# Performance work log

Measured on AMD Instinct MI355X. Metric: run time of the kernel, lower is better.

The kernel has to match this reference:

```python
import jax, jax.numpy as jnp
from jax import lax
import numpy as np

N, C, H, W = 8, 32, 64, 64
KS, NB = 7, 6            # kernel_size, num_bases
TB = (KS // 2) * NB      # total_bases = 18
BC = TB * NB             # bc_dim = 108
INTER = max(64, BC // 2) # 64
OUT = 64
PAD = KS // 2
EPS = 1e-5


def conv3x3(x, w, b):
    # x: (N,Cin,H,W), w: (Cout,Cin,3,3)
    y = lax.conv_general_dilated(x, w, (1, 1), [(1, 1), (1, 1)],
                                 dimension_numbers=('NCHW', 'OIHW', 'NCHW'))
    return y + b[None, :, None, None]


def batchnorm(x, g, b):
    # training-mode BN: batch stats over (N,H,W)
    mu = jnp.mean(x, axis=(0, 2, 3), keepdims=True)
    var = jnp.var(x, axis=(0, 2, 3), keepdims=True)
    return (x - mu) * lax.rsqrt(var + EPS) * g[None, :, None, None] + b[None, :, None, None]


def setup_inputs() -> dict:
    key = jax.random.key(0)
    ks = jax.random.split(key, 12)
    s = 0.05
    # random bases as in get_random_bases: (TB, KS*KS), zero-mean-ish rows
    f = jax.random.normal(ks[0], (TB, KS * KS), dtype=jnp.float32)
    bases = f - jnp.mean(f, axis=1, keepdims=True) / jnp.std(f, axis=1, keepdims=True)
    return {
        'x': jax.random.normal(ks[1], (N, C, H, W), dtype=jnp.float32),
        'conv1_w': jax.random.normal(ks[2], (INTER, C, 3, 3), dtype=jnp.float32) * s,
        'conv1_b': jax.random.normal(ks[3], (INTER,), dtype=jnp.float32) * s,
        'bn1_g': jnp.ones((INTER,), jnp.float32),
        'bn1_b': jnp.zeros((INTER,), jnp.float32),
        'conv2_w': jax.random.normal(ks[4], (BC, INTER, 3, 3), dtype=jnp.float32) * s,
        'conv2_b': jax.random.normal(ks[5], (BC,), dtype=jnp.float32) * s,
        'bn2_g': jnp.ones((BC,), jnp.float32),
        'bn2_b': jnp.zeros((BC,), jnp.float32),
        'bases': bases,
        'out_w': jax.random.normal(ks[6], (OUT, C * NB), dtype=jnp.float32) * s,
        'out_b': jax.random.normal(ks[7], (OUT,), dtype=jnp.float32) * s,
    }


def reference(x, conv1_w, conv1_b, bn1_g, bn1_b, conv2_w, conv2_b,
              bn2_g, bn2_b, bases, out_w, out_b):
    # bases_net: conv3x3 -> BN -> tanh -> conv3x3 -> BN -> tanh
    h = jnp.tanh(batchnorm(conv3x3(x, conv1_w, conv1_b), bn1_g, bn1_b))
    coef = jnp.tanh(batchnorm(conv3x3(h, conv2_w, conv2_b), bn2_g, bn2_b))
    # (N, BC, H, W) -> (N, NB, TB, H, W) -> (N, H, W, NB, TB)
    coef = coef.reshape(N, NB, TB, H, W).transpose(0, 3, 4, 1, 2)
    # atoms: (coef[...,None] * bases).sum(-2).transpose(-1,-2) => (N,H,W,KS^2,NB)
    atoms = jnp.einsum('nhwmt,tk->nhwkm', coef, bases)
    # unfold: channel-major (C, ks, ks) flattened, matching F.unfold
    patches = lax.conv_general_dilated_patches(
        x, (KS, KS), (1, 1), [(PAD, PAD), (PAD, PAD)],
        dimension_numbers=('NCHW', 'OIHW', 'NCHW'))  # (N, C*KS*KS, H, W)
    patches = patches.reshape(N, C, KS * KS, H, W)
    # per-pixel contraction over ks^2: (N,H,W,C,NB)
    bases_out = jnp.einsum('nckhw,nhwkm->nhwcm', patches, atoms)
    bases_out = bases_out.reshape(N, H, W, C * NB)
    out = jnp.einsum('nhwd,od->nohw', bases_out, out_w) + out_b[None, :, None, None]
    return out
```

## Files before the change

### kernel.cpp

```cpp
#include <hip/hip_runtime.h>
#include <hip/hip_bf16.h>

#define N_ 8
#define C_ 32
#define H_ 64
#define W_ 64
#define HW_ (H_*W_)
#define NHW_ (N_*HW_)
#define INTER_ 64
#define BC_ 108
#define KS_ 7
#define K2_ (KS_*KS_)
#define NB_ 6
#define TB_ 18
#define OUT_ 64
#define DDIM_ (C_*NB_)
#define P2CH_ 288

typedef __attribute__((ext_vector_type(8))) short short8;
typedef __attribute__((ext_vector_type(4))) float f32x4;
typedef __attribute__((ext_vector_type(2))) float f32x2;

__device__ __forceinline__ unsigned short f2bf(float f) {
    union { float f; unsigned u; } v; v.f = f;
    unsigned r = v.u + 0x7fffu + ((v.u >> 16) & 1u);
    return (unsigned short)(r >> 16);
}
__device__ __forceinline__ float bf2f(unsigned short h) {
    return __uint_as_float((unsigned int)h << 16);
}

__device__ __forceinline__ short8 frag4(const unsigned int* p) {
    union { unsigned int u[4]; short8 s; } v;
    v.u[0] = p[0]; v.u[1] = p[1]; v.u[2] = p[2]; v.u[3] = p[3];
    return v.s;
}

template<int TP0, int NTP>
__device__ __forceinline__ void pconv_pass(const float (*sx)[44],
                                           const float* __restrict__ bases,
                                           unsigned int* __restrict__ P2,
                                           int n, int c, int r0, int rb, int lane) {
    f32x2 av[NTP][4];
    #pragma unroll
    for (int tp = 0; tp < NTP; tp++)
        #pragma unroll
        for (int rr = 0; rr < 4; rr++) av[tp][rr] = (f32x2){0.f, 0.f};

    #pragma unroll 1
    for (int kx = 0; kx < 7; kx++) {
        float rw[12];
        const float* sp = &sx[lane + kx][rb];
        #pragma unroll
        for (int qq = 0; qq < 3; qq++) {
            float4 r4 = *(const float4*)(sp + qq * 4);
            rw[qq * 4 + 0] = r4.x; rw[qq * 4 + 1] = r4.y;
            rw[qq * 4 + 2] = r4.z; rw[qq * 4 + 3] = r4.w;
        }
        #pragma unroll
        for (int tp = 0; tp < NTP; tp++) {
            #pragma unroll
            for (int ky = 0; ky < 7; ky++) {
                f32x2 w2;
                w2.x = bases[(2 * (TP0 + tp)) * K2_ + ky * 7 + kx];
                w2.y = bases[(2 * (TP0 + tp) + 1) * K2_ + ky * 7 + kx];
                #pragma unroll
                for (int rr = 0; rr < 4; rr++) {
                    float xv = rw[rr + ky];
                    f32x2 xv2 = (f32x2){xv, xv};
                    av[tp][rr] += xv2 * w2;
                }
            }
        }
    }

    #pragma unroll
    for (int tp = 0; tp < NTP; tp++)
        #pragma unroll
        for (int rr = 0; rr < 4; rr++) {
            int gr = r0 + rb + rr;
            unsigned int pk = (unsigned int)f2bf(av[tp][rr].x) |
                              ((unsigned int)f2bf(av[tp][rr].y) << 16);
            P2[(((size_t)n * P2CH_ + (TP0 + tp) * 32 + c) << 12) + (gr << 6) + lane] = pk;
        }
}

__global__ __launch_bounds__(256) void k_prep(const float* __restrict__ w1,
                                              const float* __restrict__ w2,
                                              const float* __restrict__ ow,
                                              unsigned short* __restrict__ wb1,
                                              unsigned short* __restrict__ wb2,
                                              unsigned short* __restrict__ wbp,
                                              float* __restrict__ pz) {
    int bid = blockIdx.x, t = threadIdx.x;
    if (bid < 72) {
        int i = bid * 256 + t;
        int ci = i & 31, co = (i >> 5) & 63, s = i >> 11;
        wb1[i] = f2bf(w1[((co << 5) + ci) * 9 + s]);
    } else if (bid < 360) {
        int i = (bid - 72) * 256 + t;
        int ci = i & 63, co = (i >> 6) & 127, s = i >> 13;
        unsigned short v = 0;
        if (co < BC_) v = f2bf(w2[((co << 6) + ci) * 9 + s]);
        wb2[i] = v;
    } else if (bid < 408) {
        int i = (bid - 360) * 256 + t;
        if (i < OUT_ * DDIM_) {
            float v = ow[i];
            unsigned short hi = f2bf(v);
            wbp[i] = hi;
            wbp[OUT_ * DDIM_ + i] = f2bf(v - bf2f(hi));
        }
    } else {
        for (int i = t; i < (INTER_ + BC_) * 8 * 2; i += 256) pz[i] = 0.f;
    }
}

__global__ __launch_bounds__(256) void k_front(const float* __restrict__ x,
                                               const float* __restrict__ bases,
                                               const unsigned short* __restrict__ wb1,
                                               const float* __restrict__ b1,
                                               unsigned int* __restrict__ P2,
                                               float* __restrict__ y1,
                                               float2* __restrict__ part1) {
    __shared__ __align__(16) char smem[16896];
    int bid = blockIdx.x, t = threadIdx.x;

    if (bid < 1024) {
        float (*sx)[44] = (float(*)[44])smem;
        int rq = bid & 3;
        int c  = (bid >> 2) & 31;
        int n  = bid >> 7;
        int lane = t & 63, wv = t >> 6;
        int r0 = rq << 4;

        const float* xc = x + (((size_t)n * C_ + c) << 12);
        #pragma unroll
        for (int j = 0; j < 6; j++) {
            int p = wv + 4 * j;
            if (p < 22) {
                int grow = r0 - 3 + p;
                bool rowok = (grow >= 0 && grow < H_);
                int wx = lane - 3;
                float v = 0.f;
                if (rowok && wx >= 0) v = xc[(grow << 6) + wx];
                sx[lane][p] = v;
                if (lane < 6) {
                    int wx2 = 61 + lane;
                    float v2 = 0.f;
                    if (rowok && wx2 < W_) v2 = xc[(grow << 6) + wx2];
                    sx[64 + lane][p] = v2;
                }
            }
        }
        __syncthreads();

        int rb = wv * 4;
        pconv_pass<0, 5>(sx, bases, P2, n, c, r0, rb, lane);
        pconv_pass<5, 4>(sx, bases, P2, n, c, r0, rb, lane);
    } else {
        unsigned short* sx1 = (unsigned short*)smem;
        float* sbp = (float*)(sx1 + 198 * 40);

        int cid = bid - 1024;
        int n = cid >> 7;
        int rem = cid & 127;
        int co0 = (rem & 1) << 5;
        int h0 = rem >> 1;
        int lane = t & 63, wv = t >> 6;
        int q = lane >> 4, n15 = lane & 15;

        for (int e = t; e < 1536; e += 256) {
            int c = e & 31, rc4 = e >> 5;
            int r = rc4 >> 4, cq = rc4 & 15;
            int hh = h0 - 1 + r;
            bool rok = (hh >= 0 && hh < H_);
            float4 v = {0.f, 0.f, 0.f, 0.f};
            if (rok) v = *(const float4*)(x + (((size_t)n * C_ + c) << 12) + (hh << 6) + cq * 4);
            unsigned short* d = sx1 + (r * 66 + 1 + cq * 4) * 40 + c;
            d[0]   = f2bf(v.x);
            d[40]  = f2bf(v.y);
            d[80]  = f2bf(v.z);
            d[120] = f2bf(v.w);
        }
        if (t < 96) {
            int c = t & 31, r = t >> 5;
            sx1[(r * 66 + 0) * 40 + c] = 0;
            sx1[(r * 66 + 65) * 40 + c] = 0;
        }
        __syncthreads();

        f32x4 acc[2];
        acc[0] = (f32x4){0.f, 0.f, 0.f, 0.f};
        acc[1] = (f32x4){0.f, 0.f, 0.f, 0.f};
        #pragma unroll
        for (int s = 0; s < 9; s++) {
            int dy = s / 3, dx = s % 3;
            short8 bfr = *(const short8*)(sx1 + (dy * 66 + wv * 16 + n15 + dx) * 40 + q * 8);
            #pragma unroll
            for (int mt = 0; mt < 2; mt++) {
                short8 afr = *(const short8*)(wb1 + s * 2048 + (co0 + mt * 16 + n15) * 32 + q * 8);
                acc[mt] = __builtin_amdgcn_mfma_f32_16x16x32_bf16(afr, bfr, acc[mt], 0, 0, 0);
            }
        }

        int wcol = wv * 16 + n15;
        float sa[2][4], sa2[2][4];
        #pragma unroll
        for (int mt = 0; mt < 2; mt++)
            #pragma unroll
            for (int reg = 0; reg < 4; reg++) {
                int co = co0 + mt * 16 + q * 4 + reg;
                float v = acc[mt][reg] + b1[co];
                y1[(((size_t)n * INTER_ + co) << 12) + (h0 << 6) + wcol] = v;
                sa[mt][reg] = v; sa2[mt][reg] = v * v;
            }
        #pragma unroll
        for (int mt = 0; mt < 2; mt++)
            #pragma unroll
            for (int reg = 0; reg < 4; reg++) {
                float s = sa[mt][reg], s2 = sa2[mt][reg];
                #pragma unroll
                for (int off = 1; off < 16; off <<= 1) {
                    s += __shfl_xor(s, off);
                    s2 += __shfl_xor(s2, off);
                }
                if (n15 == 0) {
                    int cl = mt * 16 + q * 4 + reg;
                    sbp[wv * 64 + cl * 2] = s;
                    sbp[wv * 64 + cl * 2 + 1] = s2;
                }
            }
        __syncthreads();
        if (t < 32) {
            float s = 0.f, s2 = 0.f;
            #pragma unroll
            for (int w = 0; w < 4; w++) { s += sbp[w * 64 + t * 2]; s2 += sbp[w * 64 + t * 2 + 1]; }
            atomicAdd(&part1[((co0 + t) << 3) + n].x, s);
            atomicAdd(&part1[((co0 + t) << 3) + n].y, s2);
        }
    }
}

template<int CIN, int COG, int ROWS, int WPAD, int NCOQ>
__global__ __launch_bounds__(256) void k_conv3(const unsigned short* __restrict__ xb,
                                               const unsigned short* __restrict__ wb,
                                               const float* __restrict__ bias,
                                               float* __restrict__ y,
                                               float2* __restrict__ part,
                                               int COUT_real) {
    constexpr int CPAD = CIN + 8;
    constexpr int NSLC = (ROWS + 2) * 66;
    constexpr int MT = COG / 16;
    constexpr int NTW = ROWS;
    constexpr int KSTEPS = CIN / 32;
    __shared__ unsigned short sx[NSLC * CPAD];
    __shared__ unsigned short sw[9 * COG * CPAD];
    __shared__ float sbp[4][COG * 2];

    int bid = blockIdx.x;
    int coq = bid % NCOQ;
    int rp = (bid / NCOQ) % (H_ / ROWS);
    int n = bid / (NCOQ * (H_ / ROWS));
    int h0 = rp * ROWS;
    int co0 = coq * COG;
    int t = threadIdx.x;
    int lane = t & 63, wv = t >> 6;
    int q = lane >> 4, n15 = lane & 15;

    {
        const unsigned int* xg = (const unsigned int*)xb + (size_t)n * HW_ * (CIN / 2);
        unsigned int* sxd = (unsigned int*)sx;
        constexpr int DW = CIN / 2;
        constexpr int DWPT = DW / 8;
        int part_ = t & 7;
        for (int sl = (t >> 3); sl < NSLC; sl += 32) {
            int r = sl / 66, col = sl % 66;
            int hh = h0 - 1 + r, ww = col - 1;
            unsigned int v[DWPT];
            #pragma unroll
            for (int i = 0; i < DWPT; i++) v[i] = 0;
            if (hh >= 0 && hh < H_ && ww >= 0 && ww < W_) {
                const unsigned int* gp = xg + (size_t)(hh * W_ + ww) * DW + part_ * DWPT;
                #pragma unroll
                for (int i = 0; i < DWPT; i++) v[i] = gp[i];
            }
            unsigned int* d = sxd + sl * (CPAD / 2) + part_ * DWPT;
            #pragma unroll
            for (int i = 0; i < DWPT; i++) d[i] = v[i];
        }
    }
    {
        const unsigned int* wg = (const unsigned int*)wb;
        unsigned int* swd = (unsigned int*)sw;
        constexpr int TOT = 9 * COG * (CIN / 2);
        for (int e = t; e < TOT; e += 256) {
            int s_co = e / (CIN / 2), cw = e % (CIN / 2);
            int s = s_co / COG, co = s_co % COG;
            swd[s_co * (CPAD / 2) + cw] = wg[((size_t)s * WPAD + co0 + co) * (CIN / 2) + cw];
        }
    }
    __syncthreads();

    f32x4 acc[NTW][MT];
    #pragma unroll
    for (int a = 0; a < NTW; a++)
        #pragma unroll
        for (int m = 0; m < MT; m++) acc[a][m] = (f32x4){0.f, 0.f, 0.f, 0.f};

    #pragma unroll
    for (int s = 0; s < 9; s++) {
        int dy = s / 3, dx = s % 3;
        #pragma unroll
        for (int kc = 0; kc < KSTEPS; kc++) {
            int ci0 = kc * 32;
            short8 bfr[NTW];
            #pragma unroll
            for (int ntl = 0; ntl < NTW; ntl++) {
                int nt = wv * NTW + ntl;
                int r_out = nt >> 2, col0 = (nt & 3) * 16;
                bfr[ntl] = *(const short8*)(sx + ((r_out + dy) * 66 + col0 + n15 + dx) * CPAD + ci0 + q * 8);
            }
            #pragma unroll
            for (int mt = 0; mt < MT; mt++) {
                short8 afr = *(const short8*)(sw + ((s * COG) + mt * 16 + n15) * CPAD + ci0 + q * 8);
                #pragma unroll
                for (int ntl = 0; ntl < NTW; ntl++)
                    acc[ntl][mt] = __builtin_amdgcn_mfma_f32_16x16x32_bf16(afr, bfr[ntl], acc[ntl][mt], 0, 0, 0);
            }
        }
    }

    float sacc[MT][4], sacc2[MT][4];
    #pragma unroll
    for (int mt = 0; mt < MT; mt++)
        #pragma unroll
        for (int reg = 0; reg < 4; reg++) { sacc[mt][reg] = 0.f; sacc2[mt][reg] = 0.f; }

    #pragma unroll
    for (int ntl = 0; ntl < NTW; ntl++) {
        int nt = wv * NTW + ntl;
        int h = h0 + (nt >> 2), wcol = (nt & 3) * 16 + n15;
        #pragma unroll
        for (int mt = 0; mt < MT; mt++) {
            #pragma unroll
            for (int reg = 0; reg < 4; reg++) {
                int co = co0 + mt * 16 + q * 4 + reg;
                if (co < COUT_real) {
                    float v = acc[ntl][mt][reg] + bias[co];
                    y[(((size_t)n * COUT_real + co) << 12) + h * W_ + wcol] = v;
                    sacc[mt][reg] += v;
                    sacc2[mt][reg] += v * v;
                }
            }
        }
    }

    #pragma unroll
    for (int mt = 0; mt < MT; mt++)
        #pragma unroll
        for (int reg = 0; reg < 4; reg++) {
            float s = sacc[mt][reg], s2 = sacc2[mt][reg];
            #pragma unroll
            for (int off = 1; off < 16; off <<= 1) {
                s += __shfl_xor(s, off);
                s2 += __shfl_xor(s2, off);
            }
            if (n15 == 0) {
                int cl = mt * 16 + q * 4 + reg;
                sbp[wv][cl * 2] = s;
                sbp[wv][cl * 2 + 1] = s2;
            }
        }
    __syncthreads();
    if (t < COG) {
        float s = 0.f, s2 = 0.f;
        #pragma unroll
        for (int w2 = 0; w2 < 4; w2++) { s += sbp[w2][t * 2]; s2 += sbp[w2][t * 2 + 1]; }
        int co = co0 + t;
        if (co < COUT_real) {
            atomicAdd(&part[(co << 3) + n].x, s);
            atomicAdd(&part[(co << 3) + n].y, s2);
        }
    }
}

__global__ __launch_bounds__(256) void k_bntr(const float* __restrict__ y1,
                                              const float2* __restrict__ part,
                                              const float* __restrict__ g,
                                              const float* __restrict__ bb,
                                              unsigned short* __restrict__ y1b) {
    __shared__ unsigned short sT[64 * 68];
    __shared__ float scs[INTER_], shs[INTER_];
    int bid = blockIdx.x, t = threadIdx.x;
    int n = bid >> 6, hw0 = (bid << 6) & 4095;
    if (t < INTER_) {
        float s = 0.f, s2 = 0.f;
        #pragma unroll
        for (int j = 0; j < 8; j++) { float2 p = part[t * 8 + j]; s += p.x; s2 += p.y; }
        float mu = s / (float)NHW_, var = s2 / (float)NHW_ - mu * mu;
        float sc = g[t] * rsqrtf(var + 1e-5f);
        scs[t] = sc; shs[t] = bb[t] - mu * sc;
    }
    __syncthreads();
    for (int i = t; i < 4096; i += 256) {
        int c = i >> 6, px = i & 63;
        float v = y1[(((size_t)n * INTER_ + c) << 12) + hw0 + px];
        sT[px * 68 + c] = f2bf(tanhf(v * scs[c] + shs[c]));
    }
    __syncthreads();
    unsigned int* yd = (unsigned int*)y1b;
    for (int i = t; i < 2048; i += 256) {
        int px = i >> 5, cw = i & 31;
        unsigned int lo = sT[px * 68 + cw * 2], hi = sT[px * 68 + cw * 2 + 1];
        yd[(((size_t)n << 12) + hw0 + px) * 32 + cw] = lo | (hi << 16);
    }
}

#define YPAD_ 97
__global__ __launch_bounds__(256) void k_ytail(const float* __restrict__ y2,
                                               const float2* __restrict__ part,
                                               const float* __restrict__ g,
                                               const float* __restrict__ bb,
                                               const unsigned int* __restrict__ P2,
                                               const unsigned short* __restrict__ wbp,
                                               const float* __restrict__ out_b,
                                               float* __restrict__ out) {
    __shared__ float scs[BC_], shs[BC_];
    __shared__ float cfs[BC_][32];
    __shared__ unsigned int sYh[32 * YPAD_];
    __shared__ unsigned int sYl[32 * YPAD_];

    int bid = blockIdx.x;
    int n = bid >> 7, px0 = (bid & 127) << 5;
    int t = threadIdx.x;

    int px = t & 31, cg = t >> 5;
    unsigned int u[4][9];
    {
        const unsigned int* Pb = P2 + (((size_t)n * P2CH_) << 12) + px0 + px;
        #pragma unroll
        for (int cc = 0; cc < 4; cc++) {
            int c = cg * 4 + cc;
            #pragma unroll
            for (int tp = 0; tp < 9; tp++)
                u[cc][tp] = Pb[(size_t)(tp * 32 + c) << 12];
        }
    }

    if (t < BC_) {
        float s = 0.f, s2 = 0.f;
        #pragma unroll
        for (int j = 0; j < 8; j++) { float2 p = part[t * 8 + j]; s += p.x; s2 += p.y; }
        float mu = s / (float)NHW_, var = s2 / (float)NHW_ - mu * mu;
        float sc = g[t] * rsqrtf(var + 1e-5f);
        scs[t] = sc; shs[t] = bb[t] - mu * sc;
    }
    __syncthreads();

    for (int i = t; i < BC_ * 32; i += 256) {
        int ch = i >> 5, pxx = i & 31;
        float v = y2[(((size_t)n * BC_ + ch) << 12) + px0 + pxx];
        cfs[ch][pxx] = tanhf(v * scs[ch] + shs[ch]);
    }
    __syncthreads();

    {
        f32x2 pv2[2][TB_];
        #pragma unroll
        for (int j = 0; j < 2; j++)
            #pragma unroll
            for (int tp = 0; tp < 9; tp++) {
                pv2[j][2 * tp].x     = __uint_as_float(u[2 * j][tp] << 16);
                pv2[j][2 * tp].y     = __uint_as_float(u[2 * j + 1][tp] << 16);
                pv2[j][2 * tp + 1].x = __uint_as_float(u[2 * j][tp] & 0xffff0000u);
                pv2[j][2 * tp + 1].y = __uint_as_float(u[2 * j + 1][tp] & 0xffff0000u);
            }
        f32x2 ym2[2][NB_];
        #pragma unroll
        for (int j = 0; j < 2; j++)
            #pragma unroll
            for (int m = 0; m < NB_; m++) ym2[j][m] = (f32x2){0.f, 0.f};
        #pragma unroll
        for (int m = 0; m < NB_; m++)
            #pragma unroll
            for (int tt = 0; tt < TB_; tt++) {
                float cfv = cfs[m * TB_ + tt][px];
                f32x2 c2 = (f32x2){cfv, cfv};
                ym2[0][m] += c2 * pv2[0][tt];
                ym2[1][m] += c2 * pv2[1][tt];
            }
        #pragma unroll
        for (int j = 0; j < 2; j++) {
            #pragma unroll
            for (int half = 0; half < 2; half++) {
                int c = cg * 4 + 2 * j + half;
                #pragma unroll
                for (int jj = 0; jj < 3; jj++) {
                    float y0 = half ? ym2[j][2 * jj].y     : ym2[j][2 * jj].x;
                    float y1v = half ? ym2[j][2 * jj + 1].y : ym2[j][2 * jj + 1].x;
                    unsigned short h0 = f2bf(y0);
                    unsigned short h1 = f2bf(y1v);
                    unsigned short l0 = f2bf(y0 - bf2f(h0));
                    unsigned short l1 = f2bf(y1v - bf2f(h1));
                    sYh[px * YPAD_ + c * 3 + jj] = (unsigned int)h0 | ((unsigned int)h1 << 16);
                    sYl[px * YPAD_ + c * 3 + jj] = (unsigned int)l0 | ((unsigned int)l1 << 16);
                }
            }
        }
    }
    __syncthreads();

    int lane = t & 63, wv = t >> 6;
    int q = lane >> 4, n15 = lane & 15;
    f32x4 acc[2];
    acc[0] = (f32x4){0.f, 0.f, 0.f, 0.f};
    acc[1] = (f32x4){0.f, 0.f, 0.f, 0.f};
    #pragma unroll
    for (int ks = 0; ks < 6; ks++) {
        short8 ah = *(const short8*)(wbp + (wv * 16 + n15) * DDIM_ + ks * 32 + q * 8);
        short8 al = *(const short8*)(wbp + OUT_ * DDIM_ + (wv * 16 + n15) * DDIM_ + ks * 32 + q * 8);
        #pragma unroll
        for (int nt = 0; nt < 2; nt++) {
            short8 bh = frag4(sYh + (nt * 16 + n15) * YPAD_ + ks * 16 + q * 4);
            short8 bl = frag4(sYl + (nt * 16 + n15) * YPAD_ + ks * 16 + q * 4);
            acc[nt] = __builtin_amdgcn_mfma_f32_16x16x32_bf16(ah, bh, acc[nt], 0, 0, 0);
            acc[nt] = __builtin_amdgcn_mfma_f32_16x16x32_bf16(ah, bl, acc[nt], 0, 0, 0);
            acc[nt] = __builtin_amdgcn_mfma_f32_16x16x32_bf16(al, bh, acc[nt], 0, 0, 0);
        }
    }
    #pragma unroll
    for (int nt = 0; nt < 2; nt++)
        #pragma unroll
        for (int reg = 0; reg < 4; reg++) {
            int o = wv * 16 + q * 4 + reg;
            out[(((size_t)n * OUT_ + o) << 12) + px0 + nt * 16 + n15] = acc[nt][reg] + out_b[o];
        }
}

extern "C" void kernel_launch(void* const* d_in, const int* in_sizes, int n_in,
                              void* d_out, int out_size, void* d_ws, size_t ws_size,
                              hipStream_t stream) {
    const float* x       = (const float*)d_in[0];
    const float* conv1_w = (const float*)d_in[1];
    const float* conv1_b = (const float*)d_in[2];
    const float* bn1_g   = (const float*)d_in[3];
    const float* bn1_b   = (const float*)d_in[4];
    const float* conv2_w = (const float*)d_in[5];
    const float* conv2_b = (const float*)d_in[6];
    const float* bn2_g   = (const float*)d_in[7];
    const float* bn2_b   = (const float*)d_in[8];
    const float* bases   = (const float*)d_in[9];
    const float* out_w   = (const float*)d_in[10];
    const float* out_b   = (const float*)d_in[11];
    float* out = (float*)d_out;

    float* y1  = (float*)d_ws;
    float* y2  = y1 + (size_t)N_ * INTER_ * HW_;
    unsigned int* P2 = (unsigned int*)(y2 + (size_t)N_ * BC_ * HW_);
    unsigned short* xb  = (unsigned short*)(P2 + (size_t)N_ * P2CH_ * HW_);
    unsigned short* y1b = xb + (size_t)NHW_ * C_;
    unsigned short* wb1 = y1b + (size_t)NHW_ * INTER_;
    unsigned short* wb2 = wb1 + 9 * 64 * 32;
    unsigned short* wbp = wb2 + 9 * 128 * 64;
    float2* part1 = (float2*)(wbp + 2 * OUT_ * DDIM_);
    float2* part2 = part1 + INTER_ * 8;

    k_prep<<<409, 256, 0, stream>>>(conv1_w, conv2_w, out_w, wb1, wb2, wbp,
                                    (float*)part1);

    k_front<<<2048, 256, 0, stream>>>(x, bases, wb1, conv1_b, P2, y1, part1);

    k_bntr<<<512, 256, 0, stream>>>(y1, part1, bn1_g, bn1_b, y1b);

    k_conv3<INTER_, 16, 2, 128, 7><<<N_ * 32 * 7, 256, 0, stream>>>(
        y1b, wb2, conv2_b, y2, part2, BC_);

    k_ytail<<<1024, 256, 0, stream>>>(y2, (const float2*)part2, bn2_g, bn2_b,
                                      P2, wbp, out_b, out);
}
```

Before: 192.1 us.

## Split patch-conv pass across twice the blocks and pre-pack bases as float2

```diff
diff --git a/kernel.cpp b/kernel.cpp
--- a/kernel.cpp
+++ b/kernel.cpp
@@ -38,7 +38,7 @@
 
 template<int TP0, int NTP>
 __device__ __forceinline__ void pconv_pass(const float (*sx)[44],
-                                           const float* __restrict__ bases,
+                                           const float2* __restrict__ bases2,
                                            unsigned int* __restrict__ P2,
                                            int n, int c, int r0, int rb, int lane) {
     f32x2 av[NTP][4];
@@ -57,13 +57,13 @@
             rw[qq * 4 + 0] = r4.x; rw[qq * 4 + 1] = r4.y;
             rw[qq * 4 + 2] = r4.z; rw[qq * 4 + 3] = r4.w;
         }
+        const float2* bk = bases2 + kx * 63 + TP0 * 7;
         #pragma unroll
         for (int tp = 0; tp < NTP; tp++) {
             #pragma unroll
             for (int ky = 0; ky < 7; ky++) {
-                f32x2 w2;
-                w2.x = bases[(2 * (TP0 + tp)) * K2_ + ky * 7 + kx];
-                w2.y = bases[(2 * (TP0 + tp) + 1) * K2_ + ky * 7 + kx];
+                float2 w = bk[tp * 7 + ky];
+                f32x2 w2; w2.x = w.x; w2.y = w.y;
                 #pragma unroll
                 for (int rr = 0; rr < 4; rr++) {
                     float xv = rw[rr + ky];
@@ -88,9 +88,11 @@
 __global__ __launch_bounds__(256) void k_prep(const float* __restrict__ w1,
                                               const float* __restrict__ w2,
                                               const float* __restrict__ ow,
+                                              const float* __restrict__ bases,
                                               unsigned short* __restrict__ wb1,
                                               unsigned short* __restrict__ wb2,
                                               unsigned short* __restrict__ wbp,
+                                              float2* __restrict__ bases2,
                                               float* __restrict__ pz) {
     int bid = blockIdx.x, t = threadIdx.x;
     if (bid < 72) {
@@ -111,13 +113,21 @@
             wbp[i] = hi;
             wbp[OUT_ * DDIM_ + i] = f2bf(v - bf2f(hi));
         }
+    } else if (bid == 408) {
+        for (int i = t; i < (INTER_ + BC_) * 8 * 2; i += 256) pz[i] = 0.f;
     } else {
-        for (int i = t; i < (INTER_ + BC_) * 8 * 2; i += 256) pz[i] = 0.f;
+        for (int i = t; i < 7 * 9 * 7; i += 256) {
+            int kx = i / 63, r = i % 63, tp = r / 7, ky = r % 7;
+            float2 v;
+            v.x = bases[(2 * tp) * K2_ + ky * 7 + kx];
+            v.y = bases[(2 * tp + 1) * K2_ + ky * 7 + kx];
+            bases2[i] = v;
+        }
     }
 }
 
 __global__ __launch_bounds__(256) void k_front(const float* __restrict__ x,
-                                               const float* __restrict__ bases,
+                                               const float2* __restrict__ bases2,
                                                const unsigned short* __restrict__ wb1,
                                                const float* __restrict__ b1,
                                                unsigned int* __restrict__ P2,
@@ -126,11 +136,12 @@
     __shared__ __align__(16) char smem[16896];
     int bid = blockIdx.x, t = threadIdx.x;
 
-    if (bid < 1024) {
+    if (bid < 2048) {
         float (*sx)[44] = (float(*)[44])smem;
-        int rq = bid & 3;
-        int c  = (bid >> 2) & 31;
-        int n  = bid >> 7;
+        int half = bid & 1;
+        int rq = (bid >> 1) & 3;
+        int c  = (bid >> 3) & 31;
+        int n  = bid >> 8;
         int lane = t & 63, wv = t >> 6;
         int r0 = rq << 4;
 
@@ -156,13 +167,13 @@
         __syncthreads();
 
         int rb = wv * 4;
-        pconv_pass<0, 5>(sx, bases, P2, n, c, r0, rb, lane);
-        pconv_pass<5, 4>(sx, bases, P2, n, c, r0, rb, lane);
+        if (half == 0) pconv_pass<0, 5>(sx, bases2, P2, n, c, r0, rb, lane);
+        else           pconv_pass<5, 4>(sx, bases2, P2, n, c, r0, rb, lane);
     } else {
         unsigned short* sx1 = (unsigned short*)smem;
         float* sbp = (float*)(sx1 + 198 * 40);
 
-        int cid = bid - 1024;
+        int cid = bid - 2048;
         int n = cid >> 7;
         int rem = cid & 127;
         int co0 = (rem & 1) << 5;
@@ -565,11 +576,12 @@
     unsigned short* wbp = wb2 + 9 * 128 * 64;
     float2* part1 = (float2*)(wbp + 2 * OUT_ * DDIM_);
     float2* part2 = part1 + INTER_ * 8;
-
-    k_prep<<<409, 256, 0, stream>>>(conv1_w, conv2_w, out_w, wb1, wb2, wbp,
-                                    (float*)part1);
-
-    k_front<<<2048, 256, 0, stream>>>(x, bases, wb1, conv1_b, P2, y1, part1);
+    float2* bases2 = part2 + BC_ * 8;
+
+    k_prep<<<410, 256, 0, stream>>>(conv1_w, conv2_w, out_w, bases,
+                                    wb1, wb2, wbp, bases2, (float*)part1);
+
+    k_front<<<3072, 256, 0, stream>>>(x, bases2, wb1, conv1_b, P2, y1, part1);
 
     k_bntr<<<512, 256, 0, stream>>>(y1, part1, bn1_g, bn1_b, y1b);
 
```

Result: slower. 197.3 us (+2.7%).

## Compute bases-patch convolution with bf16 MFMA instead of scalar FMA

Applied to the files above, without the earlier changes.

```diff
diff --git a/kernel.cpp b/kernel.cpp
--- a/kernel.cpp
+++ b/kernel.cpp
@@ -36,61 +36,21 @@
     return v.s;
 }
 
-template<int TP0, int NTP>
-__device__ __forceinline__ void pconv_pass(const float (*sx)[44],
-                                           const float* __restrict__ bases,
-                                           unsigned int* __restrict__ P2,
-                                           int n, int c, int r0, int rb, int lane) {
-    f32x2 av[NTP][4];
-    #pragma unroll
-    for (int tp = 0; tp < NTP; tp++)
-        #pragma unroll
-        for (int rr = 0; rr < 4; rr++) av[tp][rr] = (f32x2){0.f, 0.f};
-
-    #pragma unroll 1
-    for (int kx = 0; kx < 7; kx++) {
-        float rw[12];
-        const float* sp = &sx[lane + kx][rb];
-        #pragma unroll
-        for (int qq = 0; qq < 3; qq++) {
-            float4 r4 = *(const float4*)(sp + qq * 4);
-            rw[qq * 4 + 0] = r4.x; rw[qq * 4 + 1] = r4.y;
-            rw[qq * 4 + 2] = r4.z; rw[qq * 4 + 3] = r4.w;
-        }
-        #pragma unroll
-        for (int tp = 0; tp < NTP; tp++) {
-            #pragma unroll
-            for (int ky = 0; ky < 7; ky++) {
-                f32x2 w2;
-                w2.x = bases[(2 * (TP0 + tp)) * K2_ + ky * 7 + kx];
-                w2.y = bases[(2 * (TP0 + tp) + 1) * K2_ + ky * 7 + kx];
-                #pragma unroll
-                for (int rr = 0; rr < 4; rr++) {
-                    float xv = rw[rr + ky];
-                    f32x2 xv2 = (f32x2){xv, xv};
-                    av[tp][rr] += xv2 * w2;
-                }
-            }
-        }
-    }
-
-    #pragma unroll
-    for (int tp = 0; tp < NTP; tp++)
-        #pragma unroll
-        for (int rr = 0; rr < 4; rr++) {
-            int gr = r0 + rb + rr;
-            unsigned int pk = (unsigned int)f2bf(av[tp][rr].x) |
-                              ((unsigned int)f2bf(av[tp][rr].y) << 16);
-            P2[(((size_t)n * P2CH_ + (TP0 + tp) * 32 + c) << 12) + (gr << 6) + lane] = pk;
-        }
+__device__ __forceinline__ short8 gath8(const unsigned short* p) {
+    union { unsigned short u[8]; short8 s; } v;
+    #pragma unroll
+    for (int j = 0; j < 8; j++) v.u[j] = p[j];
+    return v.s;
 }
 
 __global__ __launch_bounds__(256) void k_prep(const float* __restrict__ w1,
                                               const float* __restrict__ w2,
                                               const float* __restrict__ ow,
+                                              const float* __restrict__ bases,
                                               unsigned short* __restrict__ wb1,
                                               unsigned short* __restrict__ wb2,
                                               unsigned short* __restrict__ wbp,
+                                              unsigned short* __restrict__ basesM,
                                               float* __restrict__ pz) {
     int bid = blockIdx.x, t = threadIdx.x;
     if (bid < 72) {
@@ -111,13 +71,24 @@
             wbp[i] = hi;
             wbp[OUT_ * DDIM_ + i] = f2bf(v - bf2f(hi));
         }
+    } else if (bid == 408) {
+        for (int i = t; i < (INTER_ + BC_) * 8 * 2; i += 256) pz[i] = 0.f;
     } else {
-        for (int i = t; i < (INTER_ + BC_) * 8 * 2; i += 256) pz[i] = 0.f;
+        for (int i = t; i < 2048; i += 256) {
+            int j = i & 7, lane = (i >> 3) & 63, sk = (i >> 9) & 1, mt = i >> 10;
+            int q = lane >> 4, n15 = lane & 15;
+            int tp2 = mt * 16 + n15;
+            int ky = sk * 4 + q, kx = j;
+            unsigned short v = 0;
+            if (tp2 < TB_ && ky < 7 && kx < 7)
+                v = f2bf(bases[tp2 * K2_ + ky * 7 + kx]);
+            basesM[i] = v;
+        }
     }
 }
 
 __global__ __launch_bounds__(256) void k_front(const float* __restrict__ x,
-                                               const float* __restrict__ bases,
+                                               const unsigned short* __restrict__ basesM,
                                                const unsigned short* __restrict__ wb1,
                                                const float* __restrict__ b1,
                                                unsigned int* __restrict__ P2,
@@ -125,44 +96,77 @@
                                                float2* __restrict__ part1) {
     __shared__ __align__(16) char smem[16896];
     int bid = blockIdx.x, t = threadIdx.x;
-
-    if (bid < 1024) {
-        float (*sx)[44] = (float(*)[44])smem;
-        int rq = bid & 3;
-        int c  = (bid >> 2) & 31;
-        int n  = bid >> 7;
+    int g = bid >> 1, fr = bid & 1;
+
+    if (fr == 0) {
+        unsigned short* xt = (unsigned short*)smem;
+        int rg = g & 3;
+        int c  = (g >> 2) & 31;
+        int n  = g >> 7;
+        int h0 = rg << 4;
         int lane = t & 63, wv = t >> 6;
-        int r0 = rq << 4;
+        int q = lane >> 4, n15 = lane & 15;
 
         const float* xc = x + (((size_t)n * C_ + c) << 12);
-        #pragma unroll
-        for (int j = 0; j < 6; j++) {
-            int p = wv + 4 * j;
-            if (p < 22) {
-                int grow = r0 - 3 + p;
-                bool rowok = (grow >= 0 && grow < H_);
-                int wx = lane - 3;
-                float v = 0.f;
-                if (rowok && wx >= 0) v = xc[(grow << 6) + wx];
-                sx[lane][p] = v;
-                if (lane < 6) {
-                    int wx2 = 61 + lane;
-                    float v2 = 0.f;
-                    if (rowok && wx2 < W_) v2 = xc[(grow << 6) + wx2];
-                    sx[64 + lane][p] = v2;
+        for (int i = t; i < 23 * 72; i += 256) {
+            int r = i / 72, cl = i % 72;
+            int gr = h0 - 3 + r, gc = cl - 3;
+            float v = 0.f;
+            if (r < 22 && gr >= 0 && gr < H_ && gc >= 0 && gc < W_)
+                v = xc[(gr << 6) + gc];
+            xt[i] = f2bf(v);
+        }
+        __syncthreads();
+
+        short8 afr[2][2];
+        #pragma unroll
+        for (int mt = 0; mt < 2; mt++)
+            #pragma unroll
+            for (int sk = 0; sk < 2; sk++)
+                afr[mt][sk] = *(const short8*)(basesM + ((mt * 2 + sk) * 64 + lane) * 8);
+
+        #pragma unroll 1
+        for (int rr = 0; rr < 4; rr++) {
+            int hrow = wv * 4 + rr;
+            int h = h0 + hrow;
+            f32x4 acc[4][2];
+            #pragma unroll
+            for (int cq = 0; cq < 4; cq++) {
+                acc[cq][0] = (f32x4){0.f, 0.f, 0.f, 0.f};
+                acc[cq][1] = (f32x4){0.f, 0.f, 0.f, 0.f};
+            }
+            #pragma unroll
+            for (int sk = 0; sk < 2; sk++) {
+                const unsigned short* bp = xt + (hrow + sk * 4 + q) * 72 + n15;
+                #pragma unroll
+                for (int cq = 0; cq < 4; cq++) {
+                    short8 bfr = gath8(bp + cq * 16);
+                    acc[cq][0] = __builtin_amdgcn_mfma_f32_16x16x32_bf16(afr[0][sk], bfr, acc[cq][0], 0, 0, 0);
+                    acc[cq][1] = __builtin_amdgcn_mfma_f32_16x16x32_bf16(afr[1][sk], bfr, acc[cq][1], 0, 0, 0);
                 }
             }
-        }
-        __syncthreads();
-
-        int rb = wv * 4;
-        pconv_pass<0, 5>(sx, bases, P2, n, c, r0, rb, lane);
-        pconv_pass<5, 4>(sx, bases, P2, n, c, r0, rb, lane);
+            size_t pb = ((size_t)n * P2CH_) << 12;
+            #pragma unroll
+            for (int cq = 0; cq < 4; cq++) {
+                int col = (cq << 4) + n15;
+                unsigned int pka = (unsigned int)f2bf(acc[cq][0][0]) |
+                                   ((unsigned int)f2bf(acc[cq][0][1]) << 16);
+                unsigned int pkb = (unsigned int)f2bf(acc[cq][0][2]) |
+                                   ((unsigned int)f2bf(acc[cq][0][3]) << 16);
+                P2[pb + (((size_t)(2 * q) * 32 + c) << 12) + (h << 6) + col] = pka;
+                P2[pb + (((size_t)(2 * q + 1) * 32 + c) << 12) + (h << 6) + col] = pkb;
+                if (q == 0) {
+                    unsigned int pkc = (unsigned int)f2bf(acc[cq][1][0]) |
+                                       ((unsigned int)f2bf(acc[cq][1][1]) << 16);
+                    P2[pb + (((size_t)8 * 32 + c) << 12) + (h << 6) + col] = pkc;
+                }
+            }
+        }
     } else {
         unsigned short* sx1 = (unsigned short*)smem;
         float* sbp = (float*)(sx1 + 198 * 40);
 
-        int cid = bid - 1024;
+        int cid = g;
         int n = cid >> 7;
         int rem = cid & 127;
         int co0 = (rem & 1) << 5;
@@ -565,11 +569,12 @@
     unsigned short* wbp = wb2 + 9 * 128 * 64;
     float2* part1 = (float2*)(wbp + 2 * OUT_ * DDIM_);
     float2* part2 = part1 + INTER_ * 8;
-
-    k_prep<<<409, 256, 0, stream>>>(conv1_w, conv2_w, out_w, wb1, wb2, wbp,
-                                    (float*)part1);
-
-    k_front<<<2048, 256, 0, stream>>>(x, bases, wb1, conv1_b, P2, y1, part1);
+    unsigned short* basesM = (unsigned short*)(part2 + BC_ * 8);
+
+    k_prep<<<410, 256, 0, stream>>>(conv1_w, conv2_w, out_w, bases,
+                                    wb1, wb2, wbp, basesM, (float*)part1);
+
+    k_front<<<2048, 256, 0, stream>>>(x, basesM, wb1, conv1_b, P2, y1, part1);
 
     k_bntr<<<512, 256, 0, stream>>>(y1, part1, bn1_g, bn1_b, y1b);
 
```

After: 185.9 us. 1.03x faster.
